# Optimization experiments

Hardware: AMD Instinct MI355X
Metric: run time of the kernel (lower is better)

## Reference

```python
import jax, jax.numpy as jnp
import numpy as np

B, N, D, E = 128, 512, 256, 8192  # graphs, nodes/graph, embed_dim, edges/graph
K = int(np.ceil(0.8 * N))         # TopKPooling ratio=0.8 -> k per graph


def setup_inputs() -> dict:
    key = jax.random.key(0)
    ks = jax.random.split(key, 16)
    Ntot = B * N
    x = jax.random.normal(ks[0], (Ntot, 4), jnp.float32)
    offs = (jnp.arange(B, dtype=jnp.int32) * N)[:, None]
    src = (jax.random.randint(ks[1], (B, E), 0, N, jnp.int32) + offs).reshape(-1)
    dst = (jax.random.randint(ks[2], (B, E), 0, N, jnp.int32) + offs).reshape(-1)
    s = 0.05
    w = lambda k, shape: jax.random.normal(k, shape, jnp.float32) * s
    return {
        'x': x, 'src': src, 'dst': dst,
        'Wr1': w(ks[3], (4, D)), 'Ws1': w(ks[4], (4, D)), 'b1': jnp.zeros((D,), jnp.float32),
        'Wr2': w(ks[5], (D, D)), 'Ws2': w(ks[6], (D, D)), 'b2': jnp.zeros((D,), jnp.float32),
        'Wr3': w(ks[7], (D, D)), 'Ws3': w(ks[8], (D, D)), 'b3': jnp.zeros((D,), jnp.float32),
        'p_attn': w(ks[9], (D,)),
        'W1': w(ks[10], (2 * D, D)), 'c1': jnp.zeros((D,), jnp.float32),
        'W2': w(ks[11], (D, D // 2)), 'c2': jnp.zeros((D // 2,), jnp.float32),
        'W3': w(ks[12], (D // 2, 1)), 'c3': jnp.zeros((1,), jnp.float32),
    }


def _graph_conv(x, src, dst, Wr, Ws, b):
    # PyG GraphConv, aggr='add': out = lin_rel(sum_{j in N(i)} x_j) + lin_root(x_i)
    agg = jax.ops.segment_sum(x[src], dst, num_segments=B * N)
    return agg @ Wr + b + x @ Ws


def _gmp_gap(xb):
    # xb: [B, n, D] -> concat(global max pool, global mean pool): [B, 2D]
    return jnp.concatenate([xb.max(axis=1), xb.mean(axis=1)], axis=1)


def reference(x, src, dst, Wr1, Ws1, b1, Wr2, Ws2, b2, Wr3, Ws3, b3,
              p_attn, W1, c1, W2, c2, W3, c3):
    h = jax.nn.relu(_graph_conv(x, src, dst, Wr1, Ws1, b1))
    x1 = _gmp_gap(h.reshape(B, N, D))
    h = jax.nn.relu(_graph_conv(h, src, dst, Wr2, Ws2, b2))
    x2 = _gmp_gap(h.reshape(B, N, D))
    h = jax.nn.relu(_graph_conv(h, src, dst, Wr3, Ws3, b3))
    # TopKPooling: score = x.p/||p||; keep top-k per graph; scale by tanh(score)
    score = (h @ p_attn) / (jnp.linalg.norm(p_attn) + 1e-16)
    vals, idx = jax.lax.top_k(score.reshape(B, N), K)           # [B, K]
    hb = h.reshape(B, N, D)
    sel = jnp.take_along_axis(hb, idx[:, :, None], axis=1) * jnp.tanh(vals)[:, :, None]
    x3 = _gmp_gap(sel)
    z = x1 + x2 + x3
    z = jax.nn.relu(z @ W1 + c1)
    z = jax.nn.relu(z @ W2 + c2)  # dropout is identity in eval mode
    return jax.nn.sigmoid(z @ W3 + c3)[:, 0]
```

## Files before the change

kernel.cpp:

```cpp
#include <hip/hip_runtime.h>

typedef unsigned short u16;
typedef unsigned int u32;

#define B_GRAPHS 128
#define N_NODES  512
#define D_DIM    256
#define E_EDGES  8192
#define K_TOP    410
#define CSR_STRIDE 12288
#define LCOL 11792
#define AS 132

typedef __attribute__((ext_vector_type(8))) __bf16 bf16x8;
typedef __attribute__((ext_vector_type(4))) float  f32x4;

__device__ __forceinline__ float bf2f(u16 h) {
  union { u32 u; float f; } c; c.u = ((u32)h) << 16; return c.f;
}
__device__ __forceinline__ float u2f(u32 u) {
  union { u32 u; float f; } c; c.u = u; return c.f;
}
__device__ __forceinline__ u16 f2bf(float f) {
  union { float f; u32 u; } c; c.f = f;
  u32 u = c.u;
  u += 0x7fffu + ((u >> 16) & 1u);
  return (u16)(u >> 16);
}
__device__ __forceinline__ void async_copy16(const void* g, void* l) {
  __builtin_amdgcn_global_load_lds((const __attribute__((address_space(1))) void*)g,
                                   (__attribute__((address_space(3))) void*)l, 16, 0, 0);
}

__global__ void zero_kernel(float* __restrict__ p) {
  *(float4*)&p[(size_t)(blockIdx.x * 256 + threadIdx.x) * 4] = float4{0.f, 0.f, 0.f, 0.f};
}

__global__ void prep_kernel(const float* __restrict__ Wr2, const float* __restrict__ Ws2,
                            const float* __restrict__ Wr3, const float* __restrict__ Ws3,
                            u16* __restrict__ WT) {
  const int mat = blockIdx.y;
  const int n = blockIdx.x;
  const int k = threadIdx.x;
  const float* W = (mat == 0) ? Wr2 : (mat == 1) ? Ws2 : (mat == 2) ? Wr3 : Ws3;
  WT[((size_t)mat << 16) + ((size_t)n << 8) + k] = f2bf(W[(size_t)k * 256 + n]);
}

__global__ __launch_bounds__(256) void csr_kernel(const int* __restrict__ src,
                                                  const int* __restrict__ dst,
                                                  u16* __restrict__ csr_col,
                                                  u32* __restrict__ csr_off) {
  __shared__ u32 cnt[512];
  __shared__ u32 scan[512];
  __shared__ u32 poff[513];
  const int g = blockIdx.x, t = threadIdx.x;
  const int base = g * N_NODES, ebase = g * E_EDGES;
  for (int i = t; i < 512; i += 256) cnt[i] = 0;
  __syncthreads();
  for (int e = t; e < E_EDGES; e += 256)
    atomicAdd(&cnt[dst[ebase + e] - base], 1u);
  __syncthreads();
  for (int i = t; i < 512; i += 256) scan[i] = (cnt[i] + 7u) & ~7u;
  __syncthreads();
  #pragma unroll 1
  for (int d = 1; d < 512; d <<= 1) {
    const u32 v0 = (t >= d) ? scan[t - d] : 0u;
    const u32 v1 = scan[t + 256 - d];
    __syncthreads();
    if (t >= d) scan[t] += v0;
    scan[t + 256] += v1;
    __syncthreads();
  }
  if (t == 0) poff[0] = 0;
  for (int i = t; i < 512; i += 256) poff[i + 1] = scan[i];
  __syncthreads();
  for (int i = t; i < 513; i += 256) csr_off[(size_t)g * 513 + i] = poff[i];
  for (int i = t; i < 512; i += 256) {
    const u32 s = poff[i] + cnt[i], e2 = poff[i + 1];
    for (u32 k = s; k < e2; ++k) csr_col[(size_t)g * CSR_STRIDE + k] = 16896;
  }
  __syncthreads();
  for (int i = t; i < 512; i += 256) cnt[i] = poff[i];
  __syncthreads();
  for (int e = t; e < E_EDGES; e += 256) {
    const int d = dst[ebase + e] - base;
    const int s = src[ebase + e] - base;
    const u32 pos = atomicAdd(&cnt[d], 1u);
    csr_col[(size_t)g * CSR_STRIDE + pos] = (u16)(s * 33);
  }
}

__global__ __launch_bounds__(256) void conv1_kernel(const float* __restrict__ x,
                             const u16* __restrict__ csr_col, const u32* __restrict__ csr_off,
                             const float* __restrict__ Wr1, const float* __restrict__ Ws1,
                             const float* __restrict__ b1,
                             u16* __restrict__ H1, float* __restrict__ X1) {
  __shared__ float xs[513 * 4];
  __shared__ float aggs[N_NODES * 5];
  __shared__ __align__(16) u16 cols[CSR_STRIDE];
  __shared__ u32 offs[513];
  const int c = blockIdx.x;
  const int g = blockIdx.y;
  const int base = g * N_NODES;
  const int t = threadIdx.x;

  for (int i = t; i < N_NODES; i += 256)
    *(float4*)&xs[i * 4] = *(const float4*)&x[(size_t)(base + i) * 4];
  if (t < 4) xs[512 * 4 + t] = 0.f;
  for (int i = t; i < CSR_STRIDE / 2; i += 256)
    ((u32*)cols)[i] = ((const u32*)(csr_col + (size_t)g * CSR_STRIDE))[i];
  for (int i = t; i < 513; i += 256) offs[i] = csr_off[(size_t)g * 513 + i];
  __syncthreads();

  #pragma unroll
  for (int nn = 0; nn < 2; ++nn) {
    const int i = t * 2 + nn;
    const u32 s0 = offs[i];
    const int nb = (int)((offs[i + 1] - s0) >> 3);
    float a0 = 0.f, a1 = 0.f, a2 = 0.f, a3 = 0.f;
    for (int b = 0; b < nb; ++b) {
      const uint4 cw = *(const uint4*)&cols[s0 + (u32)b * 8];
      const u32 ww[4] = {cw.x, cw.y, cw.z, cw.w};
      #pragma unroll
      for (int q = 0; q < 4; ++q) {
        const int ca = (int)(((ww[q] & 0xffffu) * 63551u) >> 21);
        const int cb = (int)(((ww[q] >> 16) * 63551u) >> 21);
        const float4 va = *(const float4*)&xs[ca * 4];
        const float4 vb = *(const float4*)&xs[cb * 4];
        a0 += va.x + vb.x; a1 += va.y + vb.y;
        a2 += va.z + vb.z; a3 += va.w + vb.w;
      }
    }
    aggs[i * 5 + 0] = a0; aggs[i * 5 + 1] = a1;
    aggs[i * 5 + 2] = a2; aggs[i * 5 + 3] = a3;
  }
  __syncthreads();

  float wr[4], wsv[4];
  #pragma unroll
  for (int k = 0; k < 4; ++k) { wr[k] = Wr1[k * 256 + t]; wsv[k] = Ws1[k * 256 + t]; }
  const float bb = b1[t];
  float mx = 0.f, sm = 0.f;
  const int nlo = c * 256;
  for (int n = nlo; n < nlo + 256; ++n) {
    float acc = bb;
    #pragma unroll
    for (int k = 0; k < 4; ++k) acc += aggs[n * 5 + k] * wr[k] + xs[n * 4 + k] * wsv[k];
    acc = fmaxf(acc, 0.f);
    H1[(size_t)(base + n) * D_DIM + t] = f2bf(acc);
    mx = fmaxf(mx, acc);
    sm += acc;
  }
  atomicMax((int*)&X1[(size_t)g * 512 + t], __float_as_int(mx));
  atomicAdd(&X1[(size_t)g * 512 + 256 + t], sm);
}

__global__ __launch_bounds__(512) void agg_gather_kernel(const u16* __restrict__ H,
                                                         const u16* __restrict__ csr_col,
                                                         const u32* __restrict__ csr_off,
                                                         u16* __restrict__ AGG) {
  __shared__ __align__(16) u16 hs[513 * AS];
  __shared__ __align__(16) u16 cols[LCOL];
  __shared__ u32 offs[513];
  __shared__ u32 swork[512];
  const int c = blockIdx.x;
  const int g = blockIdx.y;
  const int base = g * N_NODES;
  const int t = threadIdx.x;

  #pragma unroll
  for (int p = 0; p < 32; ++p) {
    const int flat = p * 512 + t;
    const int row = flat >> 5, q = flat & 31;
    *(uint2*)&hs[row * AS + q * 4] =
        *(const uint2*)&H[(size_t)(base + row) * D_DIM + c * 128 + q * 4];
  }
  if (t < 33) *(uint2*)&hs[512 * AS + t * 4] = uint2{0u, 0u};
  {
    const u32* colsw = (const u32*)(csr_col + (size_t)g * CSR_STRIDE);
    #pragma unroll
    for (int p = 0; p < 12; ++p) {
      const int i = p * 512 + t;
      if (i < (LCOL - 8) / 2) ((u32*)cols)[i] = colsw[i];
    }
  }
  if (t < 8) cols[LCOL - 8 + t] = 16896;
  for (int i = t; i < 513; i += 512) offs[i] = csr_off[(size_t)g * 513 + i];
  __syncthreads();

  const int w = t >> 6, lane = t & 63;
  {
    const int row = (w << 6) + lane;
    const u32 s0 = offs[row];
    const u32 nb = (offs[row + 1] - s0) >> 3;
    u32 key = (nb << 16) | (u32)row;
    #pragma unroll
    for (int k = 2; k <= 64; k <<= 1) {
      #pragma unroll
      for (int jj = k >> 1; jj > 0; jj >>= 1) {
        const u32 o = (u32)__shfl_xor((int)key, jj);
        const bool up = ((lane & k) == 0);
        const bool lower = ((lane & jj) == 0);
        const u32 mn = min(key, o), mx = max(key, o);
        key = (up == lower) ? mn : mx;
      }
    }
    swork[(w << 6) + lane] = key;
  }
  __syncthreads();

  const int h2 = lane >> 5, fl = lane & 31;
  const int i0w = w << 6;
  const u32 padu = (u32)(LCOL - 8 + h2 * 4);
  const u32 h2o = (u32)(h2 * 4);
  #pragma unroll 1
  for (int j = 0; j < 16; ++j) {
    const uint4 kw = *(const uint4*)&swork[i0w + j * 4];
    const int r0 = (int)(kw.x & 0xffffu), r1 = (int)(kw.y & 0xffffu);
    const int r2 = (int)(kw.z & 0xffffu), r3 = (int)(kw.w & 0xffffu);
    const int n0b = (int)(kw.x >> 16), n1b = (int)(kw.y >> 16);
    const int n2b = (int)(kw.z >> 16), n3b = (int)(kw.w >> 16);
    const int nbmax = n3b;
    u32 cu0 = offs[r0] + h2o, cu1 = offs[r1] + h2o;
    u32 cu2 = offs[r2] + h2o, cu3 = offs[r3] + h2o;
    float a[4][4];
    #pragma unroll
    for (int q = 0; q < 4; ++q) { a[q][0] = 0.f; a[q][1] = 0.f; a[q][2] = 0.f; a[q][3] = 0.f; }
    #pragma unroll 1
    for (int b = 0; b < nbmax; ++b) {
      const u32 u0 = (b < n0b) ? cu0 : padu;
      const u32 u1 = (b < n1b) ? cu1 : padu;
      const u32 u2 = (b < n2b) ? cu2 : padu;
      const u32 u3 = (b < n3b) ? cu3 : padu;
      const u32 uu[4] = {u0, u1, u2, u3};
      #pragma unroll
      for (int q = 0; q < 4; ++q) {
        const uint2 cw = *(const uint2*)&cols[uu[q]];
        const int e0 = (int)(cw.x & 0xffffu), e1 = (int)(cw.x >> 16);
        const int e2 = (int)(cw.y & 0xffffu), e3 = (int)(cw.y >> 16);
        const uint2 d0 = *(const uint2*)&hs[(u32)(e0 + fl) << 2];
        const uint2 d1 = *(const uint2*)&hs[(u32)(e1 + fl) << 2];
        const uint2 d2 = *(const uint2*)&hs[(u32)(e2 + fl) << 2];
        const uint2 d3 = *(const uint2*)&hs[(u32)(e3 + fl) << 2];
        a[q][0] += (u2f(d0.x << 16) + u2f(d1.x << 16)) + (u2f(d2.x << 16) + u2f(d3.x << 16));
        a[q][1] += (u2f(d0.x & 0xffff0000u) + u2f(d1.x & 0xffff0000u))
                 + (u2f(d2.x & 0xffff0000u) + u2f(d3.x & 0xffff0000u));
        a[q][2] += (u2f(d0.y << 16) + u2f(d1.y << 16)) + (u2f(d2.y << 16) + u2f(d3.y << 16));
        a[q][3] += (u2f(d0.y & 0xffff0000u) + u2f(d1.y & 0xffff0000u))
                 + (u2f(d2.y & 0xffff0000u) + u2f(d3.y & 0xffff0000u));
      }
      cu0 += 8; cu1 += 8; cu2 += 8; cu3 += 8;
    }
    const int rw[4] = {r0, r1, r2, r3};
    #pragma unroll
    for (int q = 0; q < 4; ++q) {
      const float v0 = a[q][0] + __shfl_xor(a[q][0], 32);
      const float v1 = a[q][1] + __shfl_xor(a[q][1], 32);
      const float v2 = a[q][2] + __shfl_xor(a[q][2], 32);
      const float v3 = a[q][3] + __shfl_xor(a[q][3], 32);
      if (h2 == 0) {
        uint2 o;
        o.x = (u32)f2bf(v0) | ((u32)f2bf(v1) << 16);
        o.y = (u32)f2bf(v2) | ((u32)f2bf(v3) << 16);
        *(uint2*)&AGG[(size_t)(base + rw[q]) * D_DIM + c * 128 + fl * 4] = o;
      }
    }
  }
}

__global__ __launch_bounds__(256) void gemm_kernel(const u16* __restrict__ Amat,
                                                   const u16* __restrict__ Hmat,
                                                   const u16* __restrict__ WrT,
                                                   const u16* __restrict__ WsT,
                                                   const float* __restrict__ bias,
                                                   u16* __restrict__ Hout,
                                                   float* __restrict__ x2pool,
                                                   float* __restrict__ score,
                                                   const float* __restrict__ pvec) {
  __shared__ __align__(16) u16 At[2][128 * 32];
  __shared__ __align__(16) u16 Bt[2][128 * 32];
  const int m0 = blockIdx.x * 128;
  const int n0 = blockIdx.y * 128;
  const int t = threadIdx.x;
  const int wid = t >> 6, lane = t & 63;
  const int wm = wid >> 1, wn = wid & 1;
  const int r16 = lane & 15, q0 = lane >> 4;

  f32x4 acc[4][4];
  const f32x4 zero = {0.f, 0.f, 0.f, 0.f};
  #pragma unroll
  for (int i = 0; i < 4; ++i)
    #pragma unroll
    for (int jj = 0; jj < 4; ++jj) acc[i][jj] = zero;

  const int srow_off = lane >> 2;
  const int sq = lane & 3;

  auto stage = [&](int s) {
    const int buf = s & 1;
    const int ph = s >> 3;
    const int kk = (s & 7) * 32;
    const u16* Ain = ph ? Hmat : Amat;
    const u16* Win = ph ? WsT : WrT;
    #pragma unroll
    for (int j = 0; j < 4; ++j) {
      const int chk = wid * 4 + j;
      const int ch8 = chk & 7;
      const int r = ch8 * 16 + srow_off;
      const int qsrc = sq ^ ((r >> 1) & 3);
      if (chk < 8)
        async_copy16(&Ain[(size_t)(m0 + r) * 256 + kk + qsrc * 8], &At[buf][ch8 * 512]);
      else
        async_copy16(&Win[(size_t)(n0 + r) * 256 + kk + qsrc * 8], &Bt[buf][ch8 * 512]);
    }
  };

  stage(0);
  #pragma unroll 1
  for (int s = 0; s < 16; ++s) {
    if (s < 15) {
      stage(s + 1);
      asm volatile("s_waitcnt vmcnt(4)" ::: "memory");
    } else {
      asm volatile("s_waitcnt vmcnt(0)" ::: "memory");
    }
    __builtin_amdgcn_s_barrier();
    const int buf = s & 1;
    bf16x8 aF[4], bF[4];
    #pragma unroll
    for (int mi = 0; mi < 4; ++mi) {
      const int arow = wm * 64 + mi * 16 + r16;
      const int qs = q0 ^ ((arow >> 1) & 3);
      aF[mi] = *(const bf16x8*)&At[buf][arow * 32 + qs * 8];
    }
    #pragma unroll
    for (int ni = 0; ni < 4; ++ni) {
      const int brow = wn * 64 + ni * 16 + r16;
      const int qs = q0 ^ ((brow >> 1) & 3);
      bF[ni] = *(const bf16x8*)&Bt[buf][brow * 32 + qs * 8];
    }
    #pragma unroll
    for (int mi = 0; mi < 4; ++mi)
      #pragma unroll
      for (int ni = 0; ni < 4; ++ni)
        acc[mi][ni] = __builtin_amdgcn_mfma_f32_16x16x32_bf16(aF[mi], bF[ni],
                                                              acc[mi][ni], 0, 0, 0);
    __builtin_amdgcn_s_barrier();
  }

  const bool do_x2 = (x2pool != nullptr);
  const bool do_sc = (score != nullptr);
  float colmax[4], colsum[4], pv[4], rpart[4][4];
  #pragma unroll
  for (int ni = 0; ni < 4; ++ni) { colmax[ni] = 0.f; colsum[ni] = 0.f; pv[ni] = 0.f; }
  #pragma unroll
  for (int mi = 0; mi < 4; ++mi)
    #pragma unroll
    for (int r = 0; r < 4; ++r) rpart[mi][r] = 0.f;
  if (do_sc) {
    #pragma unroll
    for (int ni = 0; ni < 4; ++ni) pv[ni] = pvec[n0 + wn * 64 + ni * 16 + r16];
  }

  #pragma unroll
  for (int mi = 0; mi < 4; ++mi) {
    const int growb = m0 + wm * 64 + mi * 16 + q0 * 4;
    #pragma unroll
    for (int ni = 0; ni < 4; ++ni) {
      const int gcol = n0 + wn * 64 + ni * 16 + r16;
      const float bv = bias[gcol];
      #pragma unroll
      for (int r = 0; r < 4; ++r) {
        float v = acc[mi][ni][r] + bv;
        v = fmaxf(v, 0.f);
        Hout[(size_t)(growb + r) * 256 + gcol] = f2bf(v);
        colmax[ni] = fmaxf(colmax[ni], v);
        colsum[ni] += v;
        rpart[mi][r] += v * pv[ni];
      }
    }
  }

  const int gg = m0 >> 9;
  if (do_x2) {
    #pragma unroll
    for (int ni = 0; ni < 4; ++ni) {
      const int gcol = n0 + wn * 64 + ni * 16 + r16;
      float cm = colmax[ni], cs = colsum[ni];
      cm = fmaxf(cm, __shfl_xor(cm, 16));
      cm = fmaxf(cm, __shfl_xor(cm, 32));
      cs += __shfl_xor(cs, 16);
      cs += __shfl_xor(cs, 32);
      if (q0 == 0) {
        atomicMax((int*)&x2pool[(size_t)gg * 512 + gcol], __float_as_int(cm));
        atomicAdd(&x2pool[(size_t)gg * 512 + 256 + gcol], cs);
      }
    }
  }
  if (do_sc) {
    #pragma unroll
    for (int mi = 0; mi < 4; ++mi) {
      const int growb = m0 + wm * 64 + mi * 16 + q0 * 4;
      #pragma unroll
      for (int r = 0; r < 4; ++r) {
        float sp = rpart[mi][r];
        sp += __shfl_xor(sp, 1);
        sp += __shfl_xor(sp, 2);
        sp += __shfl_xor(sp, 4);
        sp += __shfl_xor(sp, 8);
        if (r16 == 0) atomicAdd(&score[growb + r], sp);
      }
    }
  }
}

__global__ __launch_bounds__(256) void sort_kernel(const float* __restrict__ score,
                                                   const float* __restrict__ p,
                                                   u16* __restrict__ top_idx,
                                                   float* __restrict__ top_scale) {
  __shared__ float sval[N_NODES];
  __shared__ int sidx[N_NODES];
  __shared__ float wsum[4];
  const int g = blockIdx.x, t = threadIdx.x;

  float pvt = p[t];
  float sq2 = pvt * pvt;
  #pragma unroll
  for (int off = 32; off > 0; off >>= 1) sq2 += __shfl_down(sq2, off);
  if ((t & 63) == 0) wsum[t >> 6] = sq2;
  __syncthreads();
  const float inv_pn = 1.f / (sqrtf(wsum[0] + wsum[1] + wsum[2] + wsum[3]) + 1e-16f);

  for (int n = t; n < N_NODES; n += 256) {
    sval[n] = score[(size_t)g * 512 + n] * inv_pn;
    sidx[n] = n;
  }
  __syncthreads();

  for (int k = 2; k <= N_NODES; k <<= 1) {
    for (int jj = k >> 1; jj > 0; jj >>= 1) {
      const int i = ((t & ~(jj - 1)) << 1) | (t & (jj - 1));
      const int ix = i | jj;
      const bool dirDesc = ((i & k) == 0);
      const float vi = sval[i], vx = sval[ix];
      const int ii = sidx[i], ij = sidx[ix];
      const bool iAfter = (vi < vx) || (vi == vx && ii > ij);
      if (dirDesc ? iAfter : !iAfter) {
        sval[i] = vx; sval[ix] = vi;
        sidx[i] = ij; sidx[ix] = ii;
      }
      __syncthreads();
    }
  }

  for (int s = t; s < K_TOP; s += 256) {
    top_idx[(size_t)g * 416 + s] = (u16)sidx[s];
    top_scale[(size_t)g * 416 + s] = tanhf(sval[s]);
  }
}

__global__ __launch_bounds__(256) void x3_pool_kernel(const u16* __restrict__ H3,
                                                      const u16* __restrict__ top_idx,
                                                      const float* __restrict__ top_scale,
                                                      float* __restrict__ X3) {
  __shared__ u16 sidxL[416];
  __shared__ float ssclL[416];
  __shared__ float redm[32 * 65];
  __shared__ float reds[32 * 65];
  const int c = blockIdx.x;
  const int g = blockIdx.y;
  const int t = threadIdx.x;
  const int fl = t & 7, rg = t >> 3;

  for (int s = t; s < K_TOP; s += 256) {
    sidxL[s] = top_idx[(size_t)g * 416 + s];
    ssclL[s] = top_scale[(size_t)g * 416 + s];
  }
  __syncthreads();

  float mx[8], sm[8];
  #pragma unroll
  for (int j = 0; j < 8; ++j) { mx[j] = -1e30f; sm[j] = 0.f; }
  const size_t rowbase = (size_t)g * 512;
  for (int s = rg; s < K_TOP; s += 32) {
    const int row = sidxL[s];
    const float sc = ssclL[s];
    const uint4 d = *(const uint4*)&H3[(rowbase + row) * 256 + c * 64 + fl * 8];
    const u32 wv[4] = {d.x, d.y, d.z, d.w};
    #pragma unroll
    for (int q = 0; q < 4; ++q) {
      const float v0 = u2f(wv[q] << 16) * sc;
      const float v1 = u2f(wv[q] & 0xffff0000u) * sc;
      mx[q * 2] = fmaxf(mx[q * 2], v0); sm[q * 2] += v0;
      mx[q * 2 + 1] = fmaxf(mx[q * 2 + 1], v1); sm[q * 2 + 1] += v1;
    }
  }
  #pragma unroll
  for (int j = 0; j < 8; ++j) {
    redm[rg * 65 + fl * 8 + j] = mx[j];
    reds[rg * 65 + fl * 8 + j] = sm[j];
  }
  __syncthreads();
  for (int st = 16; st >= 1; st >>= 1) {
    if (rg < st) {
      #pragma unroll
      for (int j = 0; j < 8; ++j) {
        const int a = rg * 65 + fl * 8 + j, b = (rg + st) * 65 + fl * 8 + j;
        redm[a] = fmaxf(redm[a], redm[b]);
        reds[a] += reds[b];
      }
    }
    __syncthreads();
  }
  if (rg == 0) {
    #pragma unroll
    for (int j = 0; j < 8; ++j) {
      X3[(size_t)g * 512 + c * 64 + fl * 8 + j] = redm[fl * 8 + j];
      X3[(size_t)g * 512 + 256 + c * 64 + fl * 8 + j] = reds[fl * 8 + j] * (1.f / (float)K_TOP);
    }
  }
}

__global__ void mlp_kernel(const float* __restrict__ X1, const float* __restrict__ X2,
                           const float* __restrict__ X3,
                           const float* __restrict__ W1, const float* __restrict__ c1,
                           const float* __restrict__ W2, const float* __restrict__ c2,
                           const float* __restrict__ W3, const float* __restrict__ c3,
                           float* __restrict__ out) {
  __shared__ float zs[512];
  __shared__ float z1[256];
  __shared__ float z2[128];
  const int g = blockIdx.x, t = threadIdx.x;
  for (int k = t; k < 512; k += 256) {
    const float x1v = X1[(size_t)g * 512 + k];
    const float x2v = X2[(size_t)g * 512 + k];
    const float x3v = X3[(size_t)g * 512 + k];
    zs[k] = (k < 256) ? (x1v + x2v + x3v)
                      : (x1v * (1.f / 512.f) + x2v * (1.f / 512.f) + x3v);
  }
  __syncthreads();
  {
    float acc = c1[t];
    for (int k = 0; k < 512; ++k) acc += zs[k] * W1[(size_t)k * 256 + t];
    z1[t] = fmaxf(acc, 0.f);
  }
  __syncthreads();
  if (t < 128) {
    float acc = c2[t];
    for (int d = 0; d < 256; ++d) acc += z1[d] * W2[(size_t)d * 128 + t];
    z2[t] = fmaxf(acc, 0.f);
  }
  __syncthreads();
  if (t == 0) {
    float acc = c3[0];
    for (int e = 0; e < 128; ++e) acc += z2[e] * W3[e];
    out[g] = 1.f / (1.f + expf(-acc));
  }
}

extern "C" void kernel_launch(void* const* d_in, const int* in_sizes, int n_in,
                              void* d_out, int out_size, void* d_ws, size_t ws_size,
                              hipStream_t stream) {
  (void)in_sizes; (void)n_in; (void)out_size; (void)ws_size;
  const float* x   = (const float*)d_in[0];
  const int* src   = (const int*)d_in[1];
  const int* dstp  = (const int*)d_in[2];
  const float* Wr1 = (const float*)d_in[3];
  const float* Ws1 = (const float*)d_in[4];
  const float* b1  = (const float*)d_in[5];
  const float* Wr2 = (const float*)d_in[6];
  const float* Ws2 = (const float*)d_in[7];
  const float* b2  = (const float*)d_in[8];
  const float* Wr3 = (const float*)d_in[9];
  const float* Ws3 = (const float*)d_in[10];
  const float* b3  = (const float*)d_in[11];
  const float* pat = (const float*)d_in[12];
  const float* W1  = (const float*)d_in[13];
  const float* c1  = (const float*)d_in[14];
  const float* W2  = (const float*)d_in[15];
  const float* c2  = (const float*)d_in[16];
  const float* W3  = (const float*)d_in[17];
  const float* c3  = (const float*)d_in[18];
  float* out = (float*)d_out;

  char* ws = (char*)d_ws;
  u16* hA  = (u16*)(ws);
  u16* hB  = (u16*)(ws + 33554432);
  u16* AGG = (u16*)(ws + 67108864);
  u16* WT  = (u16*)(ws + 100663296);
  float* x1 = (float*)(ws + 101187584);
  float* x2 = (float*)(ws + 101449728);
  float* x3 = (float*)(ws + 101711872);
  u16* csr_col = (u16*)(ws + 101974016);
  u32* csr_off = (u32*)(ws + 105119744);
  float* score     = (float*)(ws + 101974016);
  u16* top_idx     = (u16*)(ws + 101974016 + 262144);
  float* top_scale = (float*)(ws + 101974016 + 372736);

  prep_kernel<<<dim3(256, 4), dim3(256), 0, stream>>>(Wr2, Ws2, Wr3, Ws3, WT);
  csr_kernel<<<dim3(128), dim3(256), 0, stream>>>(src, dstp, csr_col, csr_off);
  zero_kernel<<<dim3(128), dim3(256), 0, stream>>>(x1);
  conv1_kernel<<<dim3(2, 128), dim3(256), 0, stream>>>(x, csr_col, csr_off, Wr1, Ws1, b1, hA, x1);

  agg_gather_kernel<<<dim3(2, 128), dim3(512), 0, stream>>>(hA, csr_col, csr_off, AGG);
  gemm_kernel<<<dim3(512, 2), dim3(256), 0, stream>>>(AGG, hA, WT, WT + 65536, b2, hB,
                                                      x2, nullptr, nullptr);

  agg_gather_kernel<<<dim3(2, 128), dim3(512), 0, stream>>>(hB, csr_col, csr_off, AGG);
  zero_kernel<<<dim3(64), dim3(256), 0, stream>>>(score);
  gemm_kernel<<<dim3(512, 2), dim3(256), 0, stream>>>(AGG, hB, WT + 131072, WT + 196608, b3, hA,
                                                      nullptr, score, pat);

  sort_kernel<<<dim3(128), dim3(256), 0, stream>>>(score, pat, top_idx, top_scale);
  x3_pool_kernel<<<dim3(4, 128), dim3(256), 0, stream>>>(hA, top_idx, top_scale, x3);
  mlp_kernel<<<dim3(128), dim3(256), 0, stream>>>(x1, x2, x3, W1, c1, W2, c2, W3, c3, out);
}
```

Baseline: 255.0 us.

## Async-load gather tiles, software-pipeline gather loop, enlarge GEMM tile to 256 rows

The gather kernel now stages H rows and CSR columns into LDS with async global-to-LDS copies, using an unpadded 128-wide row layout and column indices encoded as shifts rather than a multiply-based decode. The inner edge loop is double-buffered so LDS loads for the next block overlap accumulation of the current one. The GEMM kernel moves to 512 threads and 256-row M tiles to improve weight reuse and halve the block count. Risks include LDS bank conflicts from dropping the row padding, higher register pressure from the double buffers, and lower occupancy from the larger GEMM tile.

```diff
diff --git a/kernel.cpp b/kernel.cpp
--- a/kernel.cpp
+++ b/kernel.cpp
@@ -9,8 +9,6 @@
 #define E_EDGES  8192
 #define K_TOP    410
 #define CSR_STRIDE 12288
-#define LCOL 11792
-#define AS 132
 
 typedef __attribute__((ext_vector_type(8))) __bf16 bf16x8;
 typedef __attribute__((ext_vector_type(4))) float  f32x4;
@@ -77,7 +75,7 @@
   for (int i = t; i < 513; i += 256) csr_off[(size_t)g * 513 + i] = poff[i];
   for (int i = t; i < 512; i += 256) {
     const u32 s = poff[i] + cnt[i], e2 = poff[i + 1];
-    for (u32 k = s; k < e2; ++k) csr_col[(size_t)g * CSR_STRIDE + k] = 16896;
+    for (u32 k = s; k < e2; ++k) csr_col[(size_t)g * CSR_STRIDE + k] = 16384;
   }
   __syncthreads();
   for (int i = t; i < 512; i += 256) cnt[i] = poff[i];
@@ -86,7 +84,7 @@
     const int d = dst[ebase + e] - base;
     const int s = src[ebase + e] - base;
     const u32 pos = atomicAdd(&cnt[d], 1u);
-    csr_col[(size_t)g * CSR_STRIDE + pos] = (u16)(s * 33);
+    csr_col[(size_t)g * CSR_STRIDE + pos] = (u16)(s << 5);
   }
 }
 
@@ -123,8 +121,8 @@
       const u32 ww[4] = {cw.x, cw.y, cw.z, cw.w};
       #pragma unroll
       for (int q = 0; q < 4; ++q) {
-        const int ca = (int)(((ww[q] & 0xffffu) * 63551u) >> 21);
-        const int cb = (int)(((ww[q] >> 16) * 63551u) >> 21);
+        const int ca = (int)((ww[q] & 0xffffu) >> 5);
+        const int cb = (int)(ww[q] >> 21);
         const float4 va = *(const float4*)&xs[ca * 4];
         const float4 vb = *(const float4*)&xs[cb * 4];
         a0 += va.x + vb.x; a1 += va.y + vb.y;
@@ -159,36 +157,33 @@
                                                          const u16* __restrict__ csr_col,
                                                          const u32* __restrict__ csr_off,
                                                          u16* __restrict__ AGG) {
-  __shared__ __align__(16) u16 hs[513 * AS];
-  __shared__ __align__(16) u16 cols[LCOL];
+  __shared__ __align__(16) u16 hs[513 * 128];
+  __shared__ __align__(16) u16 cols[CSR_STRIDE + 8];
   __shared__ u32 offs[513];
   __shared__ u32 swork[512];
   const int c = blockIdx.x;
   const int g = blockIdx.y;
   const int base = g * N_NODES;
   const int t = threadIdx.x;
-
-  #pragma unroll
-  for (int p = 0; p < 32; ++p) {
-    const int flat = p * 512 + t;
-    const int row = flat >> 5, q = flat & 31;
-    *(uint2*)&hs[row * AS + q * 4] =
-        *(const uint2*)&H[(size_t)(base + row) * D_DIM + c * 128 + q * 4];
-  }
-  if (t < 33) *(uint2*)&hs[512 * AS + t * 4] = uint2{0u, 0u};
+  const int w = t >> 6, lane = t & 63;
+
   {
-    const u32* colsw = (const u32*)(csr_col + (size_t)g * CSR_STRIDE);
-    #pragma unroll
-    for (int p = 0; p < 12; ++p) {
-      const int i = p * 512 + t;
-      if (i < (LCOL - 8) / 2) ((u32*)cols)[i] = colsw[i];
-    }
-  }
-  if (t < 8) cols[LCOL - 8 + t] = 16896;
+    const int r0w = w * 64;
+    const u16* Hsrc = &H[(size_t)(base + r0w + (lane >> 4)) * D_DIM + c * 128 + (lane & 15) * 8];
+    #pragma unroll
+    for (int i = 0; i < 16; ++i)
+      async_copy16(Hsrc + (size_t)i * 4 * D_DIM, &hs[(r0w + i * 4) * 128]);
+    const u16* Csrc = &csr_col[(size_t)g * CSR_STRIDE + w * 1536 + lane * 8];
+    #pragma unroll
+    for (int i = 0; i < 3; ++i)
+      async_copy16(Csrc + i * 512, &cols[(w * 3 + i) * 512]);
+  }
+  if (t < 32) *(uint2*)&hs[512 * 128 + t * 4] = uint2{0u, 0u};
+  if (t < 8) cols[CSR_STRIDE + t] = 16384;
   for (int i = t; i < 513; i += 512) offs[i] = csr_off[(size_t)g * 513 + i];
-  __syncthreads();
-
-  const int w = t >> 6, lane = t & 63;
+  asm volatile("s_waitcnt vmcnt(0)" ::: "memory");
+  __syncthreads();
+
   {
     const int row = (w << 6) + lane;
     const u32 s0 = offs[row];
@@ -211,37 +206,42 @@
 
   const int h2 = lane >> 5, fl = lane & 31;
   const int i0w = w << 6;
-  const u32 padu = (u32)(LCOL - 8 + h2 * 4);
+  const u32 padu = (u32)(CSR_STRIDE + h2 * 4);
   const u32 h2o = (u32)(h2 * 4);
   #pragma unroll 1
   for (int j = 0; j < 16; ++j) {
     const uint4 kw = *(const uint4*)&swork[i0w + j * 4];
-    const int r0 = (int)(kw.x & 0xffffu), r1 = (int)(kw.y & 0xffffu);
-    const int r2 = (int)(kw.z & 0xffffu), r3 = (int)(kw.w & 0xffffu);
-    const int n0b = (int)(kw.x >> 16), n1b = (int)(kw.y >> 16);
-    const int n2b = (int)(kw.z >> 16), n3b = (int)(kw.w >> 16);
-    const int nbmax = n3b;
-    u32 cu0 = offs[r0] + h2o, cu1 = offs[r1] + h2o;
-    u32 cu2 = offs[r2] + h2o, cu3 = offs[r3] + h2o;
+    const int rw[4] = {(int)(kw.x & 0xffffu), (int)(kw.y & 0xffffu),
+                       (int)(kw.z & 0xffffu), (int)(kw.w & 0xffffu)};
+    const int nb[4] = {(int)(kw.x >> 16), (int)(kw.y >> 16),
+                       (int)(kw.z >> 16), (int)(kw.w >> 16)};
+    const int nbmax = nb[3];
+    u32 cu[4];
+    #pragma unroll
+    for (int q = 0; q < 4; ++q) cu[q] = offs[rw[q]] + h2o;
     float a[4][4];
     #pragma unroll
     for (int q = 0; q < 4; ++q) { a[q][0] = 0.f; a[q][1] = 0.f; a[q][2] = 0.f; a[q][3] = 0.f; }
-    #pragma unroll 1
-    for (int b = 0; b < nbmax; ++b) {
-      const u32 u0 = (b < n0b) ? cu0 : padu;
-      const u32 u1 = (b < n1b) ? cu1 : padu;
-      const u32 u2 = (b < n2b) ? cu2 : padu;
-      const u32 u3 = (b < n3b) ? cu3 : padu;
-      const u32 uu[4] = {u0, u1, u2, u3};
+
+    uint2 dA[16], dB[16];
+    auto LOAD = [&](uint2 (&d)[16], int b) {
       #pragma unroll
       for (int q = 0; q < 4; ++q) {
-        const uint2 cw = *(const uint2*)&cols[uu[q]];
+        const u32 u = (b < nb[q]) ? (cu[q] + (u32)b * 8u) : padu;
+        const uint2 cw = *(const uint2*)&cols[u];
         const int e0 = (int)(cw.x & 0xffffu), e1 = (int)(cw.x >> 16);
         const int e2 = (int)(cw.y & 0xffffu), e3 = (int)(cw.y >> 16);
-        const uint2 d0 = *(const uint2*)&hs[(u32)(e0 + fl) << 2];
-        const uint2 d1 = *(const uint2*)&hs[(u32)(e1 + fl) << 2];
-        const uint2 d2 = *(const uint2*)&hs[(u32)(e2 + fl) << 2];
-        const uint2 d3 = *(const uint2*)&hs[(u32)(e3 + fl) << 2];
+        d[q * 4 + 0] = *(const uint2*)&hs[(u32)(e0 + fl) << 2];
+        d[q * 4 + 1] = *(const uint2*)&hs[(u32)(e1 + fl) << 2];
+        d[q * 4 + 2] = *(const uint2*)&hs[(u32)(e2 + fl) << 2];
+        d[q * 4 + 3] = *(const uint2*)&hs[(u32)(e3 + fl) << 2];
+      }
+    };
+    auto ACCUM = [&](uint2 (&d)[16]) {
+      #pragma unroll
+      for (int q = 0; q < 4; ++q) {
+        const uint2 d0 = d[q * 4 + 0], d1 = d[q * 4 + 1];
+        const uint2 d2 = d[q * 4 + 2], d3 = d[q * 4 + 3];
         a[q][0] += (u2f(d0.x << 16) + u2f(d1.x << 16)) + (u2f(d2.x << 16) + u2f(d3.x << 16));
         a[q][1] += (u2f(d0.x & 0xffff0000u) + u2f(d1.x & 0xffff0000u))
                  + (u2f(d2.x & 0xffff0000u) + u2f(d3.x & 0xffff0000u));
@@ -249,9 +249,17 @@
         a[q][3] += (u2f(d0.y & 0xffff0000u) + u2f(d1.y & 0xffff0000u))
                  + (u2f(d2.y & 0xffff0000u) + u2f(d3.y & 0xffff0000u));
       }
-      cu0 += 8; cu1 += 8; cu2 += 8; cu3 += 8;
-    }
-    const int rw[4] = {r0, r1, r2, r3};
+    };
+
+    LOAD(dA, 0);
+    #pragma unroll 1
+    for (int b = 0; b < nbmax; b += 2) {
+      if (b + 1 < nbmax) LOAD(dB, b + 1);
+      ACCUM(dA);
+      if (b + 2 < nbmax) LOAD(dA, b + 2);
+      if (b + 1 < nbmax) ACCUM(dB);
+    }
+
     #pragma unroll
     for (int q = 0; q < 4; ++q) {
       const float v0 = a[q][0] + __shfl_xor(a[q][0], 32);
@@ -268,7 +276,7 @@
   }
 }
 
-__global__ __launch_bounds__(256) void gemm_kernel(const u16* __restrict__ Amat,
+__global__ __launch_bounds__(512) void gemm_kernel(const u16* __restrict__ Amat,
                                                    const u16* __restrict__ Hmat,
                                                    const u16* __restrict__ WrT,
                                                    const u16* __restrict__ WsT,
@@ -277,9 +285,9 @@
                                                    float* __restrict__ x2pool,
                                                    float* __restrict__ score,
                                                    const float* __restrict__ pvec) {
-  __shared__ __align__(16) u16 At[2][128 * 32];
+  __shared__ __align__(16) u16 At[2][256 * 32];
   __shared__ __align__(16) u16 Bt[2][128 * 32];
-  const int m0 = blockIdx.x * 128;
+  const int m0 = blockIdx.x * 256;
   const int n0 = blockIdx.y * 128;
   const int t = threadIdx.x;
   const int wid = t >> 6, lane = t & 63;
@@ -303,15 +311,18 @@
     const u16* Ain = ph ? Hmat : Amat;
     const u16* Win = ph ? WsT : WrT;
     #pragma unroll
-    for (int j = 0; j < 4; ++j) {
-      const int chk = wid * 4 + j;
-      const int ch8 = chk & 7;
-      const int r = ch8 * 16 + srow_off;
-      const int qsrc = sq ^ ((r >> 1) & 3);
-      if (chk < 8)
-        async_copy16(&Ain[(size_t)(m0 + r) * 256 + kk + qsrc * 8], &At[buf][ch8 * 512]);
-      else
-        async_copy16(&Win[(size_t)(n0 + r) * 256 + kk + qsrc * 8], &Bt[buf][ch8 * 512]);
+    for (int j = 0; j < 3; ++j) {
+      const int chk = wid * 3 + j;
+      if (chk < 16) {
+        const int r = chk * 16 + srow_off;
+        const int qsrc = sq ^ ((r >> 1) & 3);
+        async_copy16(&Ain[(size_t)(m0 + r) * 256 + kk + qsrc * 8], &At[buf][chk * 512]);
+      } else {
+        const int ch = chk - 16;
+        const int r = ch * 16 + srow_off;
+        const int qsrc = sq ^ ((r >> 1) & 3);
+        async_copy16(&Win[(size_t)(n0 + r) * 256 + kk + qsrc * 8], &Bt[buf][ch * 512]);
+      }
     }
   };
 
@@ -320,7 +331,7 @@
   for (int s = 0; s < 16; ++s) {
     if (s < 15) {
       stage(s + 1);
-      asm volatile("s_waitcnt vmcnt(4)" ::: "memory");
+      asm volatile("s_waitcnt vmcnt(3)" ::: "memory");
     } else {
       asm volatile("s_waitcnt vmcnt(0)" ::: "memory");
     }
@@ -603,12 +614,12 @@
   conv1_kernel<<<dim3(2, 128), dim3(256), 0, stream>>>(x, csr_col, csr_off, Wr1, Ws1, b1, hA, x1);
 
   agg_gather_kernel<<<dim3(2, 128), dim3(512), 0, stream>>>(hA, csr_col, csr_off, AGG);
-  gemm_kernel<<<dim3(512, 2), dim3(256), 0, stream>>>(AGG, hA, WT, WT + 65536, b2, hB,
+  gemm_kernel<<<dim3(256, 2), dim3(512), 0, stream>>>(AGG, hA, WT, WT + 65536, b2, hB,
                                                       x2, nullptr, nullptr);
 
   agg_gather_kernel<<<dim3(2, 128), dim3(512), 0, stream>>>(hB, csr_col, csr_off, AGG);
   zero_kernel<<<dim3(64), dim3(256), 0, stream>>>(score);
-  gemm_kernel<<<dim3(512, 2), dim3(256), 0, stream>>>(AGG, hB, WT + 131072, WT + 196608, b3, hA,
+  gemm_kernel<<<dim3(256, 2), dim3(512), 0, stream>>>(AGG, hB, WT + 131072, WT + 196608, b3, hA,
                                                       nullptr, score, pat);
 
   sort_kernel<<<dim3(128), dim3(256), 0, stream>>>(score, pat, top_idx, top_scale);
```

Result: no change. 252.8 us (-0.9%).
